# Optimization experiments

Hardware: AMD Instinct MI355X
Metric: run time of the kernel (lower is better)

The kernel has to match this reference:

```python
import jax, jax.numpy as jnp
import numpy as np

Q, P = 32, 32          # output / input channels per node
N1, N2 = 64, 64        # per-dimension quadrature grid sizes (d = 2)
B = 16                 # batch
HID = 128              # MLP hidden width (kernel_layers = [128, 128])


def _mlp_K(y, x, Ws, bs):
    """Per-dimension NN kernel: K[a, c, i, j] = MLP([y_i, x_j])[a*P + c].

    Returns the Khatri-Rao component of shape (Q, P, n_out, n_in).
    """
    n_out, n_in = y.shape[0], x.shape[0]
    feats = jnp.stack([jnp.broadcast_to(y[:, None], (n_out, n_in)),
                       jnp.broadcast_to(x[None, :], (n_out, n_in))], axis=-1)  # (n_out, n_in, 2)
    h = feats
    for W, b in zip(Ws[:-1], bs[:-1]):
        h = jax.nn.gelu(h @ W + b)
    out = h @ Ws[-1] + bs[-1]  # (n_out, n_in, Q*P)
    return out.reshape(n_out, n_in, Q, P).transpose(2, 3, 0, 1)


def setup_inputs() -> dict:
    key = jax.random.key(0)
    ks = jax.random.split(key, 12)

    def w(k, shape):
        return jax.random.normal(k, shape, jnp.float32) / np.float32(np.sqrt(shape[0]))

    return {
        "u":  jax.random.normal(ks[0], (B, P * N1 * N2), jnp.float32),
        "x1": jax.random.uniform(ks[1], (N1,), jnp.float32),   # quadrature points dim 1
        "x2": jax.random.uniform(ks[2], (N2,), jnp.float32),   # quadrature points dim 2
        "w1": jax.random.uniform(ks[3], (N1,), jnp.float32) / N1,  # quadrature weights dim 1
        "w2": jax.random.uniform(ks[4], (N2,), jnp.float32) / N2,  # quadrature weights dim 2
        "k1_W0": w(ks[5], (2, HID)),    "k1_b0": jnp.zeros((HID,), jnp.float32),
        "k1_W1": w(ks[6], (HID, HID)),  "k1_b1": jnp.zeros((HID,), jnp.float32),
        "k1_W2": w(ks[7], (HID, Q * P)), "k1_b2": jnp.zeros((Q * P,), jnp.float32),
        "k2_W0": w(ks[8], (2, HID)),    "k2_b0": jnp.zeros((HID,), jnp.float32),
        "k2_W1": w(ks[9], (HID, HID)),  "k2_b1": jnp.zeros((HID,), jnp.float32),
        "k2_W2": w(ks[10], (HID, Q * P)), "k2_b2": jnp.zeros((Q * P,), jnp.float32),
    }


def reference(u, x1, x2, w1, w2,
              k1_W0, k1_b0, k1_W1, k1_b1, k1_W2, k1_b2,
              k2_W0, k2_b0, k2_W1, k2_b1, k2_W2, k2_b2):
    # Khatri-Rao components, one per spatial dimension
    K1 = _mlp_K(x1, x1, [k1_W0, k1_W1, k1_W2], [k1_b0, k1_b1, k1_b2])  # (Q, P, N1, N1)
    K2 = _mlp_K(x2, x2, [k2_W0, k2_W1, k2_W2], [k2_b0, k2_b1, k2_b2])  # (Q, P, N2, N2)

    # (I_p kron diag(w1 kron w2)) @ u^T  ==  per-channel quadrature weighting
    v = u.reshape(B, P, N1, N2)
    vw = v * w1[None, None, :, None] * w2[None, None, None, :]

    # Block (a, c) of the full kernel is K1[a, c] kron K2[a, c]; apply it as two
    # mode-products without ever materializing the (Q*N, P*N) dense matrix.
    Z1 = jnp.einsum('acij,bcjm->bacim', K1, vw)    # contract dim-1 input index j
    out = jnp.einsum('ackm,bacim->baik', K2, Z1)   # contract dim-2 index m, sum channels c
    return out.reshape(B, Q * N1 * N2)
```

## Files before the change

### kernel.cpp

```cpp
#include <hip/hip_runtime.h>
#include <cmath>

namespace {

typedef short short8 __attribute__((ext_vector_type(8)));
typedef float f32x4  __attribute__((ext_vector_type(4)));
typedef unsigned short ushort;

constexpr int HID  = 128;
constexpr int QP   = 1024;
constexpr int N    = 64;
constexpr int NPTS = 4096;
constexpr int B    = 16;
constexpr int P    = 32;
constexpr int Q    = 32;
constexpr int LDH  = 136;
constexpr int CH   = 4;
constexpr int CCH  = P / CH;

__device__ __forceinline__ ushort f2bf(float x) {
    unsigned u = __float_as_uint(x);
    u += 0x7FFF + ((u >> 16) & 1);
    return (ushort)(u >> 16);
}
__device__ __forceinline__ float bf2f(ushort b) {
    return __uint_as_float((unsigned)b << 16);
}
__device__ __forceinline__ float gelu_tanh(float x) {
    const float c0 = 0.7978845608028654f;
    const float c1 = 0.044715f;
    float inner = c0 * (x + c1 * x * x * x);
    return 0.5f * x * (1.0f + tanhf(inner));
}
__device__ __forceinline__ void gll16(const ushort* src, ushort* dst) {
    __builtin_amdgcn_global_load_lds(
        (const __attribute__((address_space(1))) unsigned int*)src,
        (__attribute__((address_space(3))) unsigned int*)dst, 16, 0, 0);
}

__global__ __launch_bounds__(256)
void prep_kernel(const float* __restrict__ W1a, const float* __restrict__ W2a,
                 const float* __restrict__ W1b, const float* __restrict__ W2b,
                 const float* __restrict__ u,
                 ushort* __restrict__ W1Th, ushort* __restrict__ W1Tl,
                 ushort* __restrict__ W2Th, ushort* __restrict__ W2Tl,
                 ushort* __restrict__ ubf)
{
    const int bid = blockIdx.x;
    if (bid < 1152) {
        const int g   = bid * 256 + threadIdx.x;
        const int dim = g / 147456;
        const int r   = g - dim * 147456;
        const float* W1 = dim ? W1b : W1a;
        const float* W2 = dim ? W2b : W2a;
        float v; ushort *dh, *dl; int idx;
        if (r < 16384) {
            const int o = r >> 7, k = r & 127;
            v = W1[k * HID + o];
            idx = dim * 16384 + r;
            dh = W1Th; dl = W1Tl;
        } else {
            const int r2 = r - 16384;
            const int o = r2 >> 7, k = r2 & 127;
            v = W2[k * QP + o];
            idx = dim * 131072 + r2;
            dh = W2Th; dl = W2Tl;
        }
        const ushort h = f2bf(v);
        const ushort l = f2bf(v - bf2f(h));
        dh[idx] = h; dl[idx] = l;
    } else {
        const int g = (bid - 1152) * 256 + threadIdx.x;
        const float4 v = reinterpret_cast<const float4*>(u)[g];
        uint2 pk;
        pk.x = (unsigned)f2bf(v.x) | ((unsigned)f2bf(v.y) << 16);
        pk.y = (unsigned)f2bf(v.z) | ((unsigned)f2bf(v.w) << 16);
        reinterpret_cast<uint2*>(ubf)[g] = pk;
    }
}

__global__ __launch_bounds__(256, 1)
void mlp_kernel(const float* __restrict__ xs1, const float* __restrict__ xs2,
                const float* __restrict__ W0a, const float* __restrict__ b0a,
                const float* __restrict__ b1a, const float* __restrict__ b2a,
                const float* __restrict__ W0b, const float* __restrict__ b0b,
                const float* __restrict__ b1b, const float* __restrict__ b2b,
                const ushort* __restrict__ W1Th, const ushort* __restrict__ W1Tl,
                const ushort* __restrict__ W2Th, const ushort* __restrict__ W2Tl,
                const float* __restrict__ qw1, const float* __restrict__ qw2,
                ushort* __restrict__ K1out, ushort* __restrict__ K2out)
{
    __shared__ ushort h0h[N * LDH];
    __shared__ ushort h1h[N * LDH];

    const int i   = blockIdx.x;
    const int dim = blockIdx.y;
    const int bz  = blockIdx.z;
    const float* xs = dim ? xs2 : xs1;
    const float* W0 = dim ? W0b : W0a;
    const float* b0 = dim ? b0b : b0a;
    const float* b1 = dim ? b1b : b1a;
    const float* b2 = dim ? b2b : b2a;
    const float* wq = dim ? qw2 : qw1;
    const ushort* w1h = W1Th + dim * 16384;
    const ushort* w1l = W1Tl + dim * 16384;
    const ushort* w2h = W2Th + dim * 131072;
    const ushort* w2l = W2Tl + dim * 131072;
    ushort* Kout = dim ? K2out : K1out;

    const int t  = threadIdx.x;
    const int w  = t >> 6;
    const int l  = t & 63;
    const int lr = l & 15;
    const int lh = l >> 4;
    const float y = xs[i];

    {
        const int ch    = t & 127;
        const int pbase = (t >> 7) * 32;
        const float wy = W0[ch], wx = W0[HID + ch], bb = b0[ch];
        for (int pp = 0; pp < 32; ++pp) {
            const int pt = pbase + pp;
            const float z = fmaf(y, wy, fmaf(xs[pt], wx, bb));
            h0h[pt * LDH + ch] = f2bf(gelu_tanh(z));
        }
    }
    __syncthreads();

    {
        #pragma unroll
        for (int cc = 0; cc < 2; ++cc) {
            const int ct = w * 2 + cc;
            const ushort* ap = w1h + (ct * 16 + lr) * HID + lh * 8;
            const ushort* aq = w1l + (ct * 16 + lr) * HID + lh * 8;
            short8 Ah[4], Al[4];
            #pragma unroll
            for (int kk = 0; kk < 4; ++kk) {
                Ah[kk] = *reinterpret_cast<const short8*>(ap + kk * 32);
                Al[kk] = *reinterpret_cast<const short8*>(aq + kk * 32);
            }
            f32x4 acc[4];
            #pragma unroll
            for (int p = 0; p < 4; ++p) acc[p] = f32x4{0.f, 0.f, 0.f, 0.f};
            #pragma unroll
            for (int kk = 0; kk < 4; ++kk) {
                short8 Bh[4];
                #pragma unroll
                for (int p = 0; p < 4; ++p)
                    Bh[p] = *reinterpret_cast<const short8*>(&h0h[(p * 16 + lr) * LDH + kk * 32 + lh * 8]);
                #pragma unroll
                for (int p = 0; p < 4; ++p)
                    acc[p] = __builtin_amdgcn_mfma_f32_16x16x32_bf16(Ah[kk], Bh[p], acc[p], 0, 0, 0);
                #pragma unroll
                for (int p = 0; p < 4; ++p)
                    acc[p] = __builtin_amdgcn_mfma_f32_16x16x32_bf16(Al[kk], Bh[p], acc[p], 0, 0, 0);
            }
            const float4 bb = *reinterpret_cast<const float4*>(&b1[ct * 16 + lh * 4]);
            #pragma unroll
            for (int p = 0; p < 4; ++p) {
                ushort hb[4];
                #pragma unroll
                for (int r = 0; r < 4; ++r) {
                    const float zv = acc[p][r] + ((const float*)&bb)[r];
                    hb[r] = f2bf(gelu_tanh(zv));
                }
                uint2 ph;
                ph.x = (unsigned)hb[0] | ((unsigned)hb[1] << 16);
                ph.y = (unsigned)hb[2] | ((unsigned)hb[3] << 16);
                *reinterpret_cast<uint2*>(&h1h[(p * 16 + lr) * LDH + ct * 16 + lh * 4]) = ph;
            }
        }
    }
    __syncthreads();

    {
        short8 Ah[4][4];
        #pragma unroll
        for (int p = 0; p < 4; ++p)
            #pragma unroll
            for (int kk = 0; kk < 4; ++kk)
                Ah[p][kk] = *reinterpret_cast<const short8*>(&h1h[(p * 16 + lr) * LDH + kk * 32 + lh * 8]);

        const int otbase = bz * 32 + w * 8;

#define LOADB(BH, BL, OT) do {                                                      \
        const ushort* _p = w2h + (size_t)((OT) * 16 + lr) * HID + lh * 8;           \
        const ushort* _q = w2l + (size_t)((OT) * 16 + lr) * HID + lh * 8;           \
        _Pragma("unroll")                                                           \
        for (int kk = 0; kk < 4; ++kk) {                                            \
            BH[kk] = *reinterpret_cast<const short8*>(_p + kk * 32);                \
            BL[kk] = *reinterpret_cast<const short8*>(_q + kk * 32);                \
        } } while (0)

#define MMTILE(BH, BL, OT) do {                                                     \
        f32x4 acc[4];                                                               \
        _Pragma("unroll")                                                           \
        for (int p = 0; p < 4; ++p) acc[p] = f32x4{0.f, 0.f, 0.f, 0.f};             \
        _Pragma("unroll")                                                           \
        for (int kk = 0; kk < 4; ++kk) {                                            \
            _Pragma("unroll")                                                       \
            for (int p = 0; p < 4; ++p)                                             \
                acc[p] = __builtin_amdgcn_mfma_f32_16x16x32_bf16(Ah[p][kk], BH[kk], acc[p], 0, 0, 0); \
            _Pragma("unroll")                                                       \
            for (int p = 0; p < 4; ++p)                                             \
                acc[p] = __builtin_amdgcn_mfma_f32_16x16x32_bf16(Ah[p][kk], BL[kk], acc[p], 0, 0, 0); \
        }                                                                           \
        const int _o = (OT) * 16 + lr;                                              \
        const float _bo = b2[_o];                                                   \
        ushort* _d = Kout + (size_t)_o * NPTS + i * 64 + lh * 4;                    \
        _Pragma("unroll")                                                           \
        for (int p = 0; p < 4; ++p) {                                               \
            const float4 _wv = *reinterpret_cast<const float4*>(wq + p * 16 + lh * 4); \
            uint2 pk;                                                               \
            pk.x = (unsigned)f2bf((acc[p][0] + _bo) * _wv.x) |                      \
                   ((unsigned)f2bf((acc[p][1] + _bo) * _wv.y) << 16);               \
            pk.y = (unsigned)f2bf((acc[p][2] + _bo) * _wv.z) |                      \
                   ((unsigned)f2bf((acc[p][3] + _bo) * _wv.w) << 16);               \
            *reinterpret_cast<uint2*>(_d + p * 16) = pk;                            \
        } } while (0)

        short8 B0h[4], B0l[4], B1h[4], B1l[4];
        LOADB(B0h, B0l, otbase + 0);
        #pragma unroll
        for (int oo = 0; oo < 8; oo += 2) {
            if (oo + 1 < 8) LOADB(B1h, B1l, otbase + oo + 1);
            MMTILE(B0h, B0l, otbase + oo);
            if (oo + 2 < 8) LOADB(B0h, B0l, otbase + oo + 2);
            MMTILE(B1h, B1l, otbase + oo + 1);
        }
#undef LOADB
#undef MMTILE
    }
}

__global__ __launch_bounds__(256, 2)
void contract_kernel(const ushort* __restrict__ ubf,
                     const ushort* __restrict__ K1,
                     const ushort* __restrict__ K2,
                     ushort* __restrict__ part)
{
    __shared__ ushort sK1[2][4096];
    __shared__ ushort sK2[2][4096];
    __shared__ ushort sZT[4][4096];

    const int id0 = blockIdx.x;
    const int id  = (id0 & 7) * 64 + (id0 >> 3);
    const int bg  = id & 3;
    const int a   = (id >> 2) & 31;
    const int ch  = id >> 7;

    const int t  = threadIdx.x;
    const int w  = t >> 6;
    const int l  = t & 63;
    const int lr = l & 15;
    const int lh = l >> 4;
    const int b  = bg * 4 + w;
    const int c0 = ch * CCH;

    ushort* zt = &sZT[w][0];
    const int sc = (((l & 7) ^ (l >> 3)) << 3);
    const int r0 = 16 * w + (l >> 3);

#define STAGE(NB, CC) do {                                                      \
        const ushort* _k1 = K1 + (((size_t)a * P + (CC)) << 12);                \
        const ushort* _k2 = K2 + (((size_t)a * P + (CC)) << 12);                \
        gll16(_k1 + (r0    ) * 64 + sc, &sK1[NB][w * 1024      ]);              \
        gll16(_k1 + (r0 + 8) * 64 + sc, &sK1[NB][w * 1024 + 512]);              \
        gll16(_k2 + (r0    ) * 64 + sc, &sK2[NB][w * 1024      ]);              \
        gll16(_k2 + (r0 + 8) * 64 + sc, &sK2[NB][w * 1024 + 512]);              \
    } while (0)

#define LOAD_UF(UF, CC) do {                                                    \
        const ushort* _up = ubf + (((size_t)b * P + (CC)) << 12);               \
        _Pragma("unroll")                                                       \
        for (int jt = 0; jt < 4; ++jt)                                          \
            _Pragma("unroll")                                                   \
            for (int kk = 0; kk < 2; ++kk)                                      \
                UF[jt][kk] = *reinterpret_cast<const short8*>(                  \
                    _up + (16 * jt + lr) * 64 + kk * 32 + lh * 8);              \
    } while (0)

#define MM1(BUF, UF) do {                                                       \
        short8 Bf[4][2];                                                        \
        _Pragma("unroll")                                                       \
        for (int kt = 0; kt < 4; ++kt)                                          \
            _Pragma("unroll")                                                   \
            for (int kk = 0; kk < 2; ++kk)                                      \
                Bf[kt][kk] = *reinterpret_cast<const short8*>(                  \
                    &sK2[BUF][(16 * kt + lr) * 64 + (((kk * 4 + lh) ^ (lr & 7)) << 3)]); \
        _Pragma("unroll")                                                       \
        for (int jt = 0; jt < 4; ++jt)                                          \
            _Pragma("unroll")                                                   \
            for (int kt = 0; kt < 4; ++kt) zacc[jt][kt] = f32x4{0.f, 0.f, 0.f, 0.f}; \
        __builtin_amdgcn_s_setprio(1);                                          \
        _Pragma("unroll")                                                       \
        for (int kk = 0; kk < 2; ++kk)                                          \
            _Pragma("unroll")                                                   \
            for (int jt = 0; jt < 4; ++jt)                                      \
                _Pragma("unroll")                                               \
                for (int kt = 0; kt < 4; ++kt)                                  \
                    zacc[jt][kt] = __builtin_amdgcn_mfma_f32_16x16x32_bf16(     \
                        UF[jt][kk], Bf[kt][kk], zacc[jt][kt], 0, 0, 0);         \
        __builtin_amdgcn_s_setprio(0);                                          \
    } while (0)

#define ZTW() do {                                                              \
        _Pragma("unroll")                                                       \
        for (int kt = 0; kt < 4; ++kt) {                                        \
            const int rbase = (16 * kt + lr) * 64;                              \
            _Pragma("unroll")                                                   \
            for (int jt = 0; jt < 4; ++jt) {                                    \
                const f32x4 z = zacc[jt][kt];                                   \
                uint2 pk;                                                       \
                pk.x = (unsigned)f2bf(z[0]) | ((unsigned)f2bf(z[1]) << 16);     \
                pk.y = (unsigned)f2bf(z[2]) | ((unsigned)f2bf(z[3]) << 16);     \
                const int g = (2 * jt + (lh >> 1)) ^ (lr & 7);                  \
                *reinterpret_cast<uint2*>(&zt[rbase + (g << 3) + (lh & 1) * 4]) = pk; \
            }                                                                   \
        }                                                                       \
    } while (0)

#define MM2(BUF) do {                                                           \
        _Pragma("unroll")                                                       \
        for (int jj = 0; jj < 2; ++jj) {                                        \
            short8 A2[4], B2[4];                                                \
            _Pragma("unroll")                                                   \
            for (int it = 0; it < 4; ++it)                                      \
                A2[it] = *reinterpret_cast<const short8*>(                      \
                    &sK1[BUF][(16 * it + lr) * 64 + (((jj * 4 + lh) ^ (lr & 7)) << 3)]); \
            _Pragma("unroll")                                                   \
            for (int kt = 0; kt < 4; ++kt)                                      \
                B2[kt] = *reinterpret_cast<const short8*>(                      \
                    &zt[(16 * kt + lr) * 64 + (((jj * 4 + lh) ^ (lr & 7)) << 3)]); \
            __builtin_amdgcn_s_setprio(1);                                      \
            _Pragma("unroll")                                                   \
            for (int it = 0; it < 4; ++it)                                      \
                _Pragma("unroll")                                               \
                for (int kt = 0; kt < 4; ++kt)                                  \
                    oacc[it][kt] = __builtin_amdgcn_mfma_f32_16x16x32_bf16(     \
                        A2[it], B2[kt], oacc[it][kt], 0, 0, 0);                 \
            __builtin_amdgcn_s_setprio(0);                                      \
        }                                                                       \
    } while (0)

    f32x4 oacc[4][4];
    #pragma unroll
    for (int it = 0; it < 4; ++it)
        #pragma unroll
        for (int kt = 0; kt < 4; ++kt) oacc[it][kt] = f32x4{0.f, 0.f, 0.f, 0.f};
    f32x4 zacc[4][4];
    short8 UFa[4][2], UFb[4][2];

    STAGE(0, c0);
    LOAD_UF(UFa, c0);
    __syncthreads();

    #pragma unroll
    for (int cc = 0; cc < CCH; ++cc) {
        const int cur = cc & 1;
        if (cc + 1 < CCH) STAGE(cur ^ 1, c0 + cc + 1);
        if (cur == 0) {
            MM1(0, UFa);
            if (cc + 1 < CCH) LOAD_UF(UFb, c0 + cc + 1);
        } else {
            MM1(1, UFb);
            if (cc + 1 < CCH) LOAD_UF(UFa, c0 + cc + 1);
        }
        ZTW();
        asm volatile("s_waitcnt lgkmcnt(0)" ::: "memory");
        __builtin_amdgcn_sched_barrier(0);
        MM2(cur);
        __syncthreads();
    }

#undef STAGE
#undef LOAD_UF
#undef MM1
#undef ZTW
#undef MM2

    ushort* pp = part + ((((size_t)ch * B + b) * Q + a) << 12);
    #pragma unroll
    for (int it = 0; it < 4; ++it)
        #pragma unroll
        for (int kt = 0; kt < 4; ++kt)
            #pragma unroll
            for (int r = 0; r < 4; ++r)
                pp[(16 * it + 4 * lh + r) * 64 + 16 * kt + lr] = f2bf(oacc[it][kt][r]);
}

__global__ __launch_bounds__(256)
void addparts_kernel(const ushort* __restrict__ part, float* __restrict__ out)
{
    const int g = blockIdx.x * 256 + threadIdx.x;
    constexpr size_t SLAB = (size_t)B * Q * NPTS / 8;
    const uint4* p = reinterpret_cast<const uint4*>(part);
    const uint4 s0 = p[g];
    const uint4 s1 = p[g + SLAB];
    const uint4 s2 = p[g + 2 * SLAB];
    const uint4 s3 = p[g + 3 * SLAB];
    float r[8];
    #pragma unroll
    for (int e = 0; e < 8; ++e) {
        const int wd = e >> 1, sh = (e & 1) * 16;
        const float v0 = bf2f((ushort)(((const unsigned*)&s0)[wd] >> sh));
        const float v1 = bf2f((ushort)(((const unsigned*)&s1)[wd] >> sh));
        const float v2 = bf2f((ushort)(((const unsigned*)&s2)[wd] >> sh));
        const float v3 = bf2f((ushort)(((const unsigned*)&s3)[wd] >> sh));
        r[e] = (v0 + v1) + (v2 + v3);
    }
    float4* o = reinterpret_cast<float4*>(out);
    o[g * 2]     = make_float4(r[0], r[1], r[2], r[3]);
    o[g * 2 + 1] = make_float4(r[4], r[5], r[6], r[7]);
}

}

extern "C" void kernel_launch(void* const* d_in, const int* in_sizes, int n_in,
                              void* d_out, int out_size, void* d_ws, size_t ws_size,
                              hipStream_t stream)
{
    const float* u     = (const float*)d_in[0];
    const float* x1    = (const float*)d_in[1];
    const float* x2    = (const float*)d_in[2];
    const float* w1    = (const float*)d_in[3];
    const float* w2    = (const float*)d_in[4];
    const float* k1W0  = (const float*)d_in[5];
    const float* k1b0  = (const float*)d_in[6];
    const float* k1W1  = (const float*)d_in[7];
    const float* k1b1  = (const float*)d_in[8];
    const float* k1W2  = (const float*)d_in[9];
    const float* k1b2  = (const float*)d_in[10];
    const float* k2W0  = (const float*)d_in[11];
    const float* k2b0  = (const float*)d_in[12];
    const float* k2W1  = (const float*)d_in[13];
    const float* k2b1  = (const float*)d_in[14];
    const float* k2W2  = (const float*)d_in[15];
    const float* k2b2  = (const float*)d_in[16];

    float* out = (float*)d_out;
    char* ws = (char*)d_ws;
    size_t off = 0;
    ushort* K1buf = (ushort*)(ws + off); off += (size_t)QP * NPTS * 2;
    ushort* K2buf = (ushort*)(ws + off); off += (size_t)QP * NPTS * 2;
    ushort* W2Th  = (ushort*)(ws + off); off += 2 * 131072 * 2;
    ushort* W2Tl  = (ushort*)(ws + off); off += 2 * 131072 * 2;
    ushort* W1Th  = (ushort*)(ws + off); off += 2 * 16384 * 2;
    ushort* W1Tl  = (ushort*)(ws + off); off += 2 * 16384 * 2;
    ushort* ubf   = (ushort*)(ws + off); off += (size_t)B * P * NPTS * 2;
    ushort* part  = (ushort*)(ws + off); off += (size_t)CH * B * Q * NPTS * 2;

    prep_kernel<<<dim3(3200), 256, 0, stream>>>(
        k1W1, k1W2, k2W1, k2W2, u, W1Th, W1Tl, W2Th, W2Tl, ubf);

    mlp_kernel<<<dim3(64, 2, 2), 256, 0, stream>>>(
        x1, x2,
        k1W0, k1b0, k1b1, k1b2,
        k2W0, k2b0, k2b1, k2b2,
        W1Th, W1Tl, W2Th, W2Tl,
        w1, w2,
        K1buf, K2buf);

    contract_kernel<<<dim3(512), 256, 0, stream>>>(ubf, K1buf, K2buf, part);

    addparts_kernel<<<dim3((B * Q * NPTS) / (256 * 8)), 256, 0, stream>>>(part, out);
}
```

Measured before the change: 63.70 us.

## Software-pipeline MM1 of next channel with MM2 using triple-buffered K1

Restructures the channel loop so the first mode-product for channel c+1 is issued before the second mode-product for channel c, with K1 triple-buffered, K2 double-buffered and the staging prefetch moved two channels ahead. It drops the explicit lgkmcnt wait and sched barrier between the two matmuls and uses a single register set for the u fragments. The aim is to overlap LDS reads and global prefetch with MFMA work across stages. In exchange it uses 8KB more LDS, which may reduce occupancy, and it depends on the ZT buffer staying valid while MM1 writes zacc.

```diff
diff --git a/kernel.cpp b/kernel.cpp
--- a/kernel.cpp
+++ b/kernel.cpp
@@ -239,7 +239,7 @@
                      const ushort* __restrict__ K2,
                      ushort* __restrict__ part)
 {
-    __shared__ ushort sK1[2][4096];
+    __shared__ ushort sK1[3][4096];
     __shared__ ushort sK2[2][4096];
     __shared__ ushort sZT[4][4096];
 
@@ -261,16 +261,16 @@
     const int sc = (((l & 7) ^ (l >> 3)) << 3);
     const int r0 = 16 * w + (l >> 3);
 
-#define STAGE(NB, CC) do {                                                      \
+#define STAGE(N1, N2, CC) do {                                                  \
         const ushort* _k1 = K1 + (((size_t)a * P + (CC)) << 12);                \
         const ushort* _k2 = K2 + (((size_t)a * P + (CC)) << 12);                \
-        gll16(_k1 + (r0    ) * 64 + sc, &sK1[NB][w * 1024      ]);              \
-        gll16(_k1 + (r0 + 8) * 64 + sc, &sK1[NB][w * 1024 + 512]);              \
-        gll16(_k2 + (r0    ) * 64 + sc, &sK2[NB][w * 1024      ]);              \
-        gll16(_k2 + (r0 + 8) * 64 + sc, &sK2[NB][w * 1024 + 512]);              \
+        gll16(_k1 + (r0    ) * 64 + sc, &sK1[N1][w * 1024      ]);              \
+        gll16(_k1 + (r0 + 8) * 64 + sc, &sK1[N1][w * 1024 + 512]);              \
+        gll16(_k2 + (r0    ) * 64 + sc, &sK2[N2][w * 1024      ]);              \
+        gll16(_k2 + (r0 + 8) * 64 + sc, &sK2[N2][w * 1024 + 512]);              \
     } while (0)
 
-#define LOAD_UF(UF, CC) do {                                                    \
+#define LOAD_UF(CC) do {                                                        \
         const ushort* _up = ubf + (((size_t)b * P + (CC)) << 12);               \
         _Pragma("unroll")                                                       \
         for (int jt = 0; jt < 4; ++jt)                                          \
@@ -280,7 +280,7 @@
                     _up + (16 * jt + lr) * 64 + kk * 32 + lh * 8);              \
     } while (0)
 
-#define MM1(BUF, UF) do {                                                       \
+#define MM1(BUF) do {                                                           \
         short8 Bf[4][2];                                                        \
         _Pragma("unroll")                                                       \
         for (int kt = 0; kt < 4; ++kt)                                          \
@@ -349,28 +349,23 @@
         #pragma unroll
         for (int kt = 0; kt < 4; ++kt) oacc[it][kt] = f32x4{0.f, 0.f, 0.f, 0.f};
     f32x4 zacc[4][4];
-    short8 UFa[4][2], UFb[4][2];
-
-    STAGE(0, c0);
-    LOAD_UF(UFa, c0);
+    short8 UF[4][2];
+
+    STAGE(0, 0, c0);
+    STAGE(1, 1, c0 + 1);
+    LOAD_UF(c0);
     __syncthreads();
+    MM1(0);
+    LOAD_UF(c0 + 1);
 
     #pragma unroll
     for (int cc = 0; cc < CCH; ++cc) {
-        const int cur = cc & 1;
-        if (cc + 1 < CCH) STAGE(cur ^ 1, c0 + cc + 1);
-        if (cur == 0) {
-            MM1(0, UFa);
-            if (cc + 1 < CCH) LOAD_UF(UFb, c0 + cc + 1);
-        } else {
-            MM1(1, UFb);
-            if (cc + 1 < CCH) LOAD_UF(UFa, c0 + cc + 1);
-        }
         ZTW();
-        asm volatile("s_waitcnt lgkmcnt(0)" ::: "memory");
-        __builtin_amdgcn_sched_barrier(0);
-        MM2(cur);
         __syncthreads();
+        if (cc + 2 < CCH) STAGE((cc + 2) % 3, (cc + 2) & 1, c0 + cc + 2);
+        if (cc + 1 < CCH) MM1((cc + 1) & 1);
+        if (cc + 2 < CCH) LOAD_UF(c0 + cc + 2);
+        MM2(cc % 3);
     }
 
 #undef STAGE
```

Result: no change. 64.47 us (+1.2%).

## Fuse partial-sum reduction into contract kernel via last-arriver atomic counter

Applied to the files above, without the earlier changes.

Removes the separate addparts kernel launch. Each contract wave writes its channel-chunk partial, then bumps a per-(b,a) atomic counter, and the fourth arriver sums the four bf16 partials and writes the fp32 output. The counters are zeroed by an extra block in the prep kernel. This saves one kernel launch and its pass over the partials, at the cost of threadfences, atomics, and a serialized tail in the last-arriving wave.

```diff
diff --git a/kernel.cpp b/kernel.cpp
--- a/kernel.cpp
+++ b/kernel.cpp
@@ -44,7 +44,7 @@
                  const float* __restrict__ u,
                  ushort* __restrict__ W1Th, ushort* __restrict__ W1Tl,
                  ushort* __restrict__ W2Th, ushort* __restrict__ W2Tl,
-                 ushort* __restrict__ ubf)
+                 ushort* __restrict__ ubf, int* __restrict__ cnt)
 {
     const int bid = blockIdx.x;
     if (bid < 1152) {
@@ -69,13 +69,16 @@
         const ushort h = f2bf(v);
         const ushort l = f2bf(v - bf2f(h));
         dh[idx] = h; dl[idx] = l;
-    } else {
+    } else if (bid < 3200) {
         const int g = (bid - 1152) * 256 + threadIdx.x;
         const float4 v = reinterpret_cast<const float4*>(u)[g];
         uint2 pk;
         pk.x = (unsigned)f2bf(v.x) | ((unsigned)f2bf(v.y) << 16);
         pk.y = (unsigned)f2bf(v.z) | ((unsigned)f2bf(v.w) << 16);
         reinterpret_cast<uint2*>(ubf)[g] = pk;
+    } else {
+        cnt[threadIdx.x] = 0;
+        cnt[256 + threadIdx.x] = 0;
     }
 }
 
@@ -237,7 +240,9 @@
 void contract_kernel(const ushort* __restrict__ ubf,
                      const ushort* __restrict__ K1,
                      const ushort* __restrict__ K2,
-                     ushort* __restrict__ part)
+                     ushort* __restrict__ part,
+                     int* __restrict__ cnt,
+                     float* __restrict__ out)
 {
     __shared__ ushort sK1[2][4096];
     __shared__ ushort sK2[2][4096];
@@ -387,31 +392,38 @@
             #pragma unroll
             for (int r = 0; r < 4; ++r)
                 pp[(16 * it + 4 * lh + r) * 64 + 16 * kt + lr] = f2bf(oacc[it][kt][r]);
-}
-
-__global__ __launch_bounds__(256)
-void addparts_kernel(const ushort* __restrict__ part, float* __restrict__ out)
-{
-    const int g = blockIdx.x * 256 + threadIdx.x;
-    constexpr size_t SLAB = (size_t)B * Q * NPTS / 8;
-    const uint4* p = reinterpret_cast<const uint4*>(part);
-    const uint4 s0 = p[g];
-    const uint4 s1 = p[g + SLAB];
-    const uint4 s2 = p[g + 2 * SLAB];
-    const uint4 s3 = p[g + 3 * SLAB];
-    float r[8];
-    #pragma unroll
-    for (int e = 0; e < 8; ++e) {
-        const int wd = e >> 1, sh = (e & 1) * 16;
-        const float v0 = bf2f((ushort)(((const unsigned*)&s0)[wd] >> sh));
-        const float v1 = bf2f((ushort)(((const unsigned*)&s1)[wd] >> sh));
-        const float v2 = bf2f((ushort)(((const unsigned*)&s2)[wd] >> sh));
-        const float v3 = bf2f((ushort)(((const unsigned*)&s3)[wd] >> sh));
-        r[e] = (v0 + v1) + (v2 + v3);
-    }
-    float4* o = reinterpret_cast<float4*>(out);
-    o[g * 2]     = make_float4(r[0], r[1], r[2], r[3]);
-    o[g * 2 + 1] = make_float4(r[4], r[5], r[6], r[7]);
+
+    __threadfence();
+    int old = 0;
+    if (l == 0) old = atomicAdd(&cnt[b * Q + a], 1);
+    old = __shfl(old, 0);
+    if (old == 3) {
+        __threadfence();
+        constexpr size_t SLAB = (size_t)B * Q * NPTS / 8;
+        const uint4* p0 = reinterpret_cast<const uint4*>(part) +
+                          (((size_t)b * Q + a) << 9);
+        float4* o4 = reinterpret_cast<float4*>(out + (((size_t)b * Q + a) << 12));
+        #pragma unroll
+        for (int e = 0; e < 8; ++e) {
+            const int g = e * 64 + l;
+            const uint4 s0 = p0[g];
+            const uint4 s1 = p0[g + SLAB];
+            const uint4 s2 = p0[g + 2 * SLAB];
+            const uint4 s3 = p0[g + 3 * SLAB];
+            float r[8];
+            #pragma unroll
+            for (int ee = 0; ee < 8; ++ee) {
+                const int wd = ee >> 1, sh = (ee & 1) * 16;
+                const float v0 = bf2f((ushort)(((const unsigned*)&s0)[wd] >> sh));
+                const float v1 = bf2f((ushort)(((const unsigned*)&s1)[wd] >> sh));
+                const float v2 = bf2f((ushort)(((const unsigned*)&s2)[wd] >> sh));
+                const float v3 = bf2f((ushort)(((const unsigned*)&s3)[wd] >> sh));
+                r[ee] = (v0 + v1) + (v2 + v3);
+            }
+            o4[g * 2]     = make_float4(r[0], r[1], r[2], r[3]);
+            o4[g * 2 + 1] = make_float4(r[4], r[5], r[6], r[7]);
+        }
+    }
 }
 
 }
@@ -449,9 +461,10 @@
     ushort* W1Tl  = (ushort*)(ws + off); off += 2 * 16384 * 2;
     ushort* ubf   = (ushort*)(ws + off); off += (size_t)B * P * NPTS * 2;
     ushort* part  = (ushort*)(ws + off); off += (size_t)CH * B * Q * NPTS * 2;
-
-    prep_kernel<<<dim3(3200), 256, 0, stream>>>(
-        k1W1, k1W2, k2W1, k2W2, u, W1Th, W1Tl, W2Th, W2Tl, ubf);
+    int*    cnt   = (int*)(ws + off);    off += 512 * sizeof(int);
+
+    prep_kernel<<<dim3(3201), 256, 0, stream>>>(
+        k1W1, k1W2, k2W1, k2W2, u, W1Th, W1Tl, W2Th, W2Tl, ubf, cnt);
 
     mlp_kernel<<<dim3(64, 2, 2), 256, 0, stream>>>(
         x1, x2,
@@ -461,7 +474,5 @@
         w1, w2,
         K1buf, K2buf);
 
-    contract_kernel<<<dim3(512), 256, 0, stream>>>(ubf, K1buf, K2buf, part);
-
-    addparts_kernel<<<dim3((B * Q * NPTS) / (256 * 8)), 256, 0, stream>>>(part, out);
-}
+    contract_kernel<<<dim3(512), 256, 0, stream>>>(ubf, K1buf, K2buf, part, cnt, out);
+}
```

Measured after the change: 171.8 us. +169.7%, slower.
